# Kernel tuning notes

Measured on AMD Instinct MI355X. Metric: run time of the kernel, lower is better.

Reference implementation:

```python
import jax, jax.numpy as jnp
import numpy as np

EPS = 1e-5
LORA_DIM = 64
LORA_SCALE = LORA_DIM ** (-0.5)
GRAD_SCALE = 0.5  # infeat_grad_scale (bp_to_unet=True path)


def _ln(x, g=None, b=None):
    mu = jnp.mean(x, axis=-1, keepdims=True)
    var = jnp.mean((x - mu) ** 2, axis=-1, keepdims=True)
    y = (x - mu) * jax.lax.rsqrt(var + EPS)
    if g is not None:
        y = y * g + b
    return y


def _grad_scale(t, s=GRAD_SCALE):
    # identity in forward, scales gradient by s in backward
    return t * s + jax.lax.stop_gradient(t) * (1.0 - s)


def setup_inputs() -> dict:
    key = jax.random.key(0)
    ks = jax.random.split(key, 8)
    B, C, H, W = 32, 1280, 32, 32
    TD, LD = 768, LORA_DIM
    inp = {}
    inp["layer_infeat"] = jax.random.normal(ks[0], (B, C, H, W), jnp.float32)
    inp["layer_inquery"] = jax.random.normal(ks[1], (B, H * W, C), jnp.float32)
    inp["token_q_emb"] = jax.random.normal(ks[2], (TD,), jnp.float32)
    # learned params
    inp["to_q_w"] = jax.random.normal(ks[3], (C, TD), jnp.float32) * (TD ** -0.5)
    inp["ln_x_g"] = jnp.ones((C,), jnp.float32)
    inp["ln_x_b"] = jnp.zeros((C,), jnp.float32)
    inp["ln_k_g"] = jnp.ones((C,), jnp.float32)
    inp["ln_k_b"] = jnp.zeros((C,), jnp.float32)
    inp["ln_q_g"] = jnp.ones((TD,), jnp.float32)
    inp["ln_q_b"] = jnp.zeros((TD,), jnp.float32)
    inp["lora_q_w"] = jax.random.normal(ks[4], (LD, C), jnp.float32) * (C ** -0.5)
    inp["lora_k_w"] = jax.random.normal(ks[5], (LD, C), jnp.float32) * (C ** -0.5)
    inp["mask"] = jax.random.randint(ks[6], (B, 1, H, W), 0, 2).astype(jnp.float32)
    return inp


def reference(layer_infeat, layer_inquery, token_q_emb, to_q_w,
              ln_x_g, ln_x_b, ln_k_g, ln_k_b, ln_q_g, ln_q_b,
              lora_q_w, lora_k_w, mask):
    B, C, H, W = layer_infeat.shape
    # flatten(2).permute(0,2,1): [B,C,H,W] -> [B, HW, C]
    x = _grad_scale(layer_infeat).reshape(B, C, H * W).transpose(0, 2, 1)
    k_in = _grad_scale(layer_inquery)
    # q = to_q(ln_q(token_q_emb[None])) -> [1, C], broadcast to [B, 1, C]
    q = _ln(token_q_emb[None, :], ln_q_g, ln_q_b) @ to_q_w.T
    q = jnp.broadcast_to(q[None], (B, 1, C))
    k = _ln(k_in, ln_k_g, ln_k_b)   # [B, HW, C]
    v = _ln(x, ln_x_g, ln_x_b)      # [B, HW, C]
    # LoRA score path (use_lora=True since lora_dim>0)
    lora_q = _ln(q) @ lora_q_w.T    # [B, 1, LD]
    lora_k = _ln(k) @ lora_k_w.T    # [B, HW, LD]
    sim = jnp.einsum('bid,bjd->bij', lora_q, lora_k) * LORA_SCALE  # [B,1,HW]
    # mask: nearest interpolation to (H,W) is identity (same size); flatten
    m = mask.reshape(B, 1, H * W) > 0
    sim = jnp.where(m, sim, -jnp.finfo(sim.dtype).max)
    attn = jax.nn.softmax(sim, axis=-1)
    fg = jnp.einsum('bij,bjd->bid', attn, v)            # [B, 1, C]
    bg = jnp.mean(v, axis=1, keepdims=True) - fg        # [B, 1, C]
    out = jnp.concatenate([fg, bg], axis=-1)            # [B, 1, 2C]
    return out[:, 0, :]                                  # [B, 2C]
```

## Files before the change

kernel.cpp:

```cpp
#include <hip/hip_runtime.h>
#include <math.h>

#define B_   32
#define CD   1280
#define HW_  1024
#define TD_  768
#define LD_  64
#define EPSF 1e-5f
#define LORA_SCALE_F 0.125f

__device__ __forceinline__ float wredSum(float a) {
#pragma unroll
  for (int o = 32; o; o >>= 1) a += __shfl_xor(a, o, 64);
  return a;
}
__device__ __forceinline__ void wred2(float& a, float& b) {
#pragma unroll
  for (int o = 32; o; o >>= 1) { a += __shfl_xor(a, o, 64); b += __shfl_xor(b, o, 64); }
}
__device__ __forceinline__ void wred3(float& a, float& b, float& c) {
#pragma unroll
  for (int o = 32; o; o >>= 1) {
    a += __shfl_xor(a, o, 64); b += __shfl_xor(b, o, 64); c += __shfl_xor(c, o, 64);
  }
}
__device__ __forceinline__ float blockSum(float v, float* red) {
  int t = threadIdx.x;
  red[t] = v; __syncthreads();
#pragma unroll
  for (int s = 128; s > 0; s >>= 1) { if (t < s) red[t] += red[t + s]; __syncthreads(); }
  float r = red[0]; __syncthreads();
  return r;
}
__device__ __forceinline__ void blockSum2(float& a, float& b, float2* red) {
  int t = threadIdx.x;
  red[t] = make_float2(a, b); __syncthreads();
#pragma unroll
  for (int s = 128; s > 0; s >>= 1) {
    if (t < s) { red[t].x += red[t + s].x; red[t].y += red[t + s].y; }
    __syncthreads();
  }
  a = red[0].x; b = red[0].y; __syncthreads();
}

__global__ __launch_bounds__(256) void kA12(const float* __restrict__ tq,
                                            const float* __restrict__ lng,
                                            const float* __restrict__ lnb,
                                            const float* __restrict__ to_q_w,
                                            float* __restrict__ q_out) {
  __shared__ float lnq[TD_];
  __shared__ float2 red[256];
  int t = threadIdx.x;
  float s = 0.f, ss = 0.f, vals[3];
#pragma unroll
  for (int k = 0; k < 3; k++) { float v = tq[t + 256 * k]; vals[k] = v; s += v; ss += v * v; }
  blockSum2(s, ss, red);
  float mu = s * (1.f / TD_);
  float r = rsqrtf(ss * (1.f / TD_) - mu * mu + EPSF);
#pragma unroll
  for (int k = 0; k < 3; k++) { int i = t + 256 * k; lnq[i] = (vals[k] - mu) * r * lng[i] + lnb[i]; }
  __syncthreads();
  int c = blockIdx.x * 4 + (t >> 6);
  int lane = t & 63;
  const float4* w4 = (const float4*)(to_q_w + (size_t)c * TD_);
  const float4* l4 = (const float4*)lnq;
  float dot = 0.f;
#pragma unroll
  for (int i = 0; i < 3; i++) {
    int f = i * 64 + lane;
    float4 w = w4[f], l = l4[f];
    dot += w.x * l.x + w.y * l.y + w.z * l.z + w.w * l.w;
  }
  dot = wredSum(dot);
  if (lane == 0) q_out[c] = dot;
}

__global__ __launch_bounds__(256) void kA3456(const float* __restrict__ q_in,
                                              const float* __restrict__ lora_q_w,
                                              const float* __restrict__ lora_k_w,
                                              float* __restrict__ w_eff) {
  __shared__ float qn[CD];
  __shared__ float lq[LD_];
  __shared__ float redS[8];
  int t = threadIdx.x;
  int wid = t >> 6, lane = t & 63;
  float s = 0.f, ss = 0.f, vals[5];
#pragma unroll
  for (int k = 0; k < 5; k++) { float v = q_in[t + 256 * k]; vals[k] = v; s += v; ss += v * v; }
  wred2(s, ss);
  if (lane == 0) { redS[wid * 2] = s; redS[wid * 2 + 1] = ss; }
  __syncthreads();
  s = redS[0] + redS[2] + redS[4] + redS[6];
  ss = redS[1] + redS[3] + redS[5] + redS[7];
  float mu = s * (1.f / CD);
  float r = rsqrtf(ss * (1.f / CD) - mu * mu + EPSF);
#pragma unroll
  for (int k = 0; k < 5; k++) { int i = t + 256 * k; qn[i] = (vals[k] - mu) * r; }
  __syncthreads();
  {
    int g = t >> 2, sub = t & 3;
    const float4* w4 = (const float4*)(lora_q_w + (size_t)g * CD);
    const float4* q4 = (const float4*)qn;
    float dot = 0.f;
#pragma unroll 8
    for (int i = 0; i < 80; i++) {
      int f = i * 4 + sub;
      float4 w = w4[f], qq = q4[f];
      dot += w.x * qq.x + w.y * qq.y + w.z * qq.z + w.w * qq.w;
    }
    dot += __shfl_xor(dot, 1, 64);
    dot += __shfl_xor(dot, 2, 64);
    if (sub == 0) lq[g] = dot;
  }
  __syncthreads();
  int c = blockIdx.x * 256 + t;
  float acc = 0.f;
#pragma unroll 8
  for (int d = 0; d < LD_; d++) acc += lq[d] * lora_k_w[(size_t)d * CD + c];
  w_eff[c] = acc;
}

__global__ __launch_bounds__(256) void kBD1(const float* __restrict__ kin,
                                            const float* __restrict__ g,
                                            const float* __restrict__ bb,
                                            const float* __restrict__ w_eff,
                                            float* __restrict__ sim,
                                            const float* __restrict__ infeat,
                                            float* __restrict__ mu_out,
                                            float* __restrict__ r_out) {
  __shared__ float4 smem[1024];
  int t = threadIdx.x;
  if (blockIdx.x < 2048) {
    float4* gs = smem;
    float4* bs = smem + 320;
    float4* ws = smem + 640;
    float* red = (float*)(smem + 960);
    float wsum = 0.f;
    for (int k = t; k < CD / 4; k += 256) {
      float4 w = ((const float4*)w_eff)[k];
      ws[k] = w;
      gs[k] = ((const float4*)g)[k];
      bs[k] = ((const float4*)bb)[k];
      wsum += w.x + w.y + w.z + w.w;
    }
    float W0 = blockSum(wsum, red);
    int wid = t >> 6, lane = t & 63;
    int gw = blockIdx.x * 4 + wid;
    for (int row = gw; row < B_ * HW_; row += 8192) {
      const float4* x4 = (const float4*)(kin + (size_t)row * CD);
      float4 xv[5];
      float s = 0.f, ss = 0.f;
#pragma unroll
      for (int i = 0; i < 5; i++) {
        float4 v = x4[i * 64 + lane];
        xv[i] = v;
        s += v.x + v.y + v.z + v.w;
        ss += v.x * v.x + v.y * v.y + v.z * v.z + v.w * v.w;
      }
      wred2(s, ss);
      float mu1 = s * (1.f / CD);
      float r1 = rsqrtf(ss * (1.f / CD) - mu1 * mu1 + EPSF);
      float s2 = 0.f, ss2 = 0.f;
#pragma unroll
      for (int i = 0; i < 5; i++) {
        int f = i * 64 + lane;
        float4 G = gs[f], Bv = bs[f], v = xv[i], kk;
        kk.x = (v.x - mu1) * r1 * G.x + Bv.x;
        kk.y = (v.y - mu1) * r1 * G.y + Bv.y;
        kk.z = (v.z - mu1) * r1 * G.z + Bv.z;
        kk.w = (v.w - mu1) * r1 * G.w + Bv.w;
        xv[i] = kk;
        s2 += kk.x + kk.y + kk.z + kk.w;
        ss2 += kk.x * kk.x + kk.y * kk.y + kk.z * kk.z + kk.w * kk.w;
      }
      wred2(s2, ss2);
      float mu2 = s2 * (1.f / CD);
      float r2 = rsqrtf(ss2 * (1.f / CD) - mu2 * mu2 + EPSF);
      float dot = 0.f;
#pragma unroll
      for (int i = 0; i < 5; i++) {
        float4 w = ws[i * 64 + lane], kk = xv[i];
        dot += w.x * kk.x + w.y * kk.y + w.z * kk.z + w.w * kk.w;
      }
      dot = wredSum(dot);
      if (lane == 0) sim[row] = LORA_SCALE_F * r2 * (dot - mu2 * W0);
    }
  } else {
    int blk = blockIdx.x - 2048;
    int tile = blk & 15, b = blk >> 4;
    int jg = t & 15;
    int slice = t >> 4;
    int j0 = tile * 64 + jg * 4;
    const float* base = infeat + (size_t)b * CD * HW_ + j0;
    float4 s = make_float4(0, 0, 0, 0), q = make_float4(0, 0, 0, 0);
    int c0 = slice * 80;
#pragma unroll 4
    for (int c = c0; c < c0 + 80; c++) {
      float4 v = *(const float4*)(base + (size_t)c * HW_);
      s.x += v.x; s.y += v.y; s.z += v.z; s.w += v.w;
      q.x += v.x * v.x; q.y += v.y * v.y; q.z += v.z * v.z; q.w += v.w * v.w;
    }
    float4* sArr = smem;
    float4* qArr = smem + 256;
    sArr[slice * 16 + jg] = s; qArr[slice * 16 + jg] = q;
    __syncthreads();
#pragma unroll
    for (int st = 8; st > 0; st >>= 1) {
      if (slice < st) {
        float4 a = sArr[slice * 16 + jg], b2 = sArr[(slice + st) * 16 + jg];
        a.x += b2.x; a.y += b2.y; a.z += b2.z; a.w += b2.w;
        sArr[slice * 16 + jg] = a;
        a = qArr[slice * 16 + jg]; b2 = qArr[(slice + st) * 16 + jg];
        a.x += b2.x; a.y += b2.y; a.z += b2.z; a.w += b2.w;
        qArr[slice * 16 + jg] = a;
      }
      __syncthreads();
    }
    if (slice == 0) {
      float4 S = sArr[jg], Q = qArr[jg], mu, r;
      mu.x = S.x * (1.f / CD); mu.y = S.y * (1.f / CD);
      mu.z = S.z * (1.f / CD); mu.w = S.w * (1.f / CD);
      r.x = rsqrtf(Q.x * (1.f / CD) - mu.x * mu.x + EPSF);
      r.y = rsqrtf(Q.y * (1.f / CD) - mu.y * mu.y + EPSF);
      r.z = rsqrtf(Q.z * (1.f / CD) - mu.z * mu.z + EPSF);
      r.w = rsqrtf(Q.w * (1.f / CD) - mu.w * mu.w + EPSF);
      int j = b * HW_ + j0;
      *(float4*)(mu_out + j) = mu;
      *(float4*)(r_out + j) = r;
    }
  }
}

__global__ __launch_bounds__(256) void kD2f(const float* __restrict__ infeat,
                                            const float* __restrict__ sim,
                                            const float* __restrict__ mask,
                                            const float* __restrict__ mu,
                                            const float* __restrict__ r,
                                            const float* __restrict__ g,
                                            const float* __restrict__ bb,
                                            float* __restrict__ out) {
  __shared__ float4 w1s[HW_ / 4], w2s[HW_ / 4];
  __shared__ float red[16];
  int t = threadIdx.x;
  int b = blockIdx.x / 40, tile = blockIdx.x % 40;
  int wid = t >> 6, lane = t & 63;

  float4 sv = ((const float4*)(sim + b * HW_))[t];
  float4 mv = ((const float4*)(mask + b * HW_))[t];
  float4 muv = ((const float4*)(mu + b * HW_))[t];
  float4 rv = ((const float4*)(r + b * HW_))[t];
  const float NEG = -3.4028235e38f;
  float se0 = mv.x > 0.f ? sv.x : NEG;
  float se1 = mv.y > 0.f ? sv.y : NEG;
  float se2 = mv.z > 0.f ? sv.z : NEG;
  float se3 = mv.w > 0.f ? sv.w : NEG;
  float m = fmaxf(fmaxf(se0, se1), fmaxf(se2, se3));
#pragma unroll
  for (int o = 32; o; o >>= 1) m = fmaxf(m, __shfl_xor(m, o, 64));
  if (lane == 0) red[wid] = m;
  __syncthreads();
  float M = fmaxf(fmaxf(red[0], red[1]), fmaxf(red[2], red[3]));
  float e0 = expf(se0 - M), e1 = expf(se1 - M), e2 = expf(se2 - M), e3 = expf(se3 - M);
  float Z = e0 + e1 + e2 + e3;
  float t1 = e0 * rv.x * muv.x + e1 * rv.y * muv.y + e2 * rv.z * muv.z + e3 * rv.w * muv.w;
  float t3 = rv.x * muv.x + rv.y * muv.y + rv.z * muv.z + rv.w * muv.w;
  wred3(Z, t1, t3);
  __syncthreads();
  if (lane == 0) { red[4 + wid * 3] = Z; red[5 + wid * 3] = t1; red[6 + wid * 3] = t3; }
  __syncthreads();
  Z  = red[4] + red[7] + red[10] + red[13];
  t1 = red[5] + red[8] + red[11] + red[14];
  t3 = red[6] + red[9] + red[12] + red[15];
  float inv = 1.f / Z;
  float s1 = t1 * inv;
  float s3 = t3 * (1.f / HW_);
  w1s[t] = make_float4(e0 * rv.x * inv, e1 * rv.y * inv, e2 * rv.z * inv, e3 * rv.w * inv);
  w2s[t] = make_float4(rv.x * (1.f / HW_), rv.y * (1.f / HW_),
                       rv.z * (1.f / HW_), rv.w * (1.f / HW_));
  __syncthreads();

#pragma unroll
  for (int k = 0; k < 8; k++) {
    int c = tile * 32 + wid * 8 + k;
    const float4* x4 = (const float4*)(infeat + (size_t)b * CD * HW_ + (size_t)c * HW_);
    float d1 = 0.f, d2 = 0.f;
#pragma unroll
    for (int i = 0; i < 4; i++) {
      int f = i * 64 + lane;
      float4 x = x4[f], a = w1s[f], w = w2s[f];
      d1 += x.x * a.x + x.y * a.y + x.z * a.z + x.w * a.w;
      d2 += x.x * w.x + x.y * w.y + x.z * w.z + x.w * w.w;
    }
    wred2(d1, d2);
    if (lane == 0) {
      float gc = g[c], bc = bb[c];
      float fg = gc * (d1 - s1) + bc;
      float vm = gc * (d2 - s3) + bc;
      out[(size_t)b * (2 * CD) + c] = fg;
      out[(size_t)b * (2 * CD) + CD + c] = vm - fg;
    }
  }
}

extern "C" void kernel_launch(void* const* d_in, const int* in_sizes, int n_in,
                              void* d_out, int out_size, void* d_ws, size_t ws_size,
                              hipStream_t stream) {
  const float* infeat  = (const float*)d_in[0];
  const float* inquery = (const float*)d_in[1];
  const float* tq      = (const float*)d_in[2];
  const float* to_q_w  = (const float*)d_in[3];
  const float* ln_x_g  = (const float*)d_in[4];
  const float* ln_x_b  = (const float*)d_in[5];
  const float* ln_k_g  = (const float*)d_in[6];
  const float* ln_k_b  = (const float*)d_in[7];
  const float* ln_q_g  = (const float*)d_in[8];
  const float* ln_q_b  = (const float*)d_in[9];
  const float* lora_q_w = (const float*)d_in[10];
  const float* lora_k_w = (const float*)d_in[11];
  const float* mask    = (const float*)d_in[12];
  float* out = (float*)d_out;

  float* ws = (float*)d_ws;
  float* q_ws    = ws;
  float* weff_ws = ws + 1280;
  float* sim_ws  = ws + 2560;
  float* mu_ws   = ws + 35328;
  float* r_ws    = ws + 68096;

  kA12<<<320, 256, 0, stream>>>(tq, ln_q_g, ln_q_b, to_q_w, q_ws);
  kA3456<<<5, 256, 0, stream>>>(q_ws, lora_q_w, lora_k_w, weff_ws);
  kBD1<<<2560, 256, 0, stream>>>(inquery, ln_k_g, ln_k_b, weff_ws, sim_ws,
                                 infeat, mu_ws, r_ws);
  kD2f<<<1280, 256, 0, stream>>>(infeat, sim_ws, mask, mu_ws, r_ws,
                                 ln_x_g, ln_x_b, out);
}
```

Before: 406.5 us.

## Interleave LN and stats blocks and process two rows per wave iteration

kBD1 now interleaves its two roles by block index (four LayerNorm-score blocks, then one infeat-stats block), so the two memory streams run concurrently instead of in two phases. Each wave now handles two rows per iteration with a fixed trip count, which doubles the loads in flight and shares the shuffle reductions between rows. The shared-memory block reduction of W0 becomes wave shuffles plus a 4-entry sum. kD2f likewise processes two channels per iteration, and launch bounds request 4 blocks per CU, which raises register pressure and risks spills.

```diff
diff --git a/kernel.cpp b/kernel.cpp
--- a/kernel.cpp
+++ b/kernel.cpp
@@ -24,13 +24,12 @@
     a += __shfl_xor(a, o, 64); b += __shfl_xor(b, o, 64); c += __shfl_xor(c, o, 64);
   }
 }
-__device__ __forceinline__ float blockSum(float v, float* red) {
-  int t = threadIdx.x;
-  red[t] = v; __syncthreads();
-#pragma unroll
-  for (int s = 128; s > 0; s >>= 1) { if (t < s) red[t] += red[t + s]; __syncthreads(); }
-  float r = red[0]; __syncthreads();
-  return r;
+__device__ __forceinline__ void wred4(float& a, float& b, float& c, float& d) {
+#pragma unroll
+  for (int o = 32; o; o >>= 1) {
+    a += __shfl_xor(a, o, 64); b += __shfl_xor(b, o, 64);
+    c += __shfl_xor(c, o, 64); d += __shfl_xor(d, o, 64);
+  }
 }
 __device__ __forceinline__ void blockSum2(float& a, float& b, float2* red) {
   int t = threadIdx.x;
@@ -120,21 +119,25 @@
   w_eff[c] = acc;
 }
 
-__global__ __launch_bounds__(256) void kBD1(const float* __restrict__ kin,
-                                            const float* __restrict__ g,
-                                            const float* __restrict__ bb,
-                                            const float* __restrict__ w_eff,
-                                            float* __restrict__ sim,
-                                            const float* __restrict__ infeat,
-                                            float* __restrict__ mu_out,
-                                            float* __restrict__ r_out) {
+__global__ __launch_bounds__(256, 4) void kBD1(const float* __restrict__ kin,
+                                               const float* __restrict__ g,
+                                               const float* __restrict__ bb,
+                                               const float* __restrict__ w_eff,
+                                               float* __restrict__ sim,
+                                               const float* __restrict__ infeat,
+                                               float* __restrict__ mu_out,
+                                               float* __restrict__ r_out) {
   __shared__ float4 smem[1024];
   int t = threadIdx.x;
-  if (blockIdx.x < 2048) {
+  int m5 = blockIdx.x % 5;
+  int d5 = blockIdx.x / 5;
+  if (m5 != 4) {
+    int kbid = d5 * 4 + m5;
     float4* gs = smem;
     float4* bs = smem + 320;
     float4* ws = smem + 640;
     float* red = (float*)(smem + 960);
+    int wid = t >> 6, lane = t & 63;
     float wsum = 0.f;
     for (int k = t; k < CD / 4; k += 256) {
       float4 w = ((const float4*)w_eff)[k];
@@ -143,50 +146,76 @@
       bs[k] = ((const float4*)bb)[k];
       wsum += w.x + w.y + w.z + w.w;
     }
-    float W0 = blockSum(wsum, red);
-    int wid = t >> 6, lane = t & 63;
-    int gw = blockIdx.x * 4 + wid;
-    for (int row = gw; row < B_ * HW_; row += 8192) {
-      const float4* x4 = (const float4*)(kin + (size_t)row * CD);
-      float4 xv[5];
-      float s = 0.f, ss = 0.f;
+    wsum = wredSum(wsum);
+    if (lane == 0) red[wid] = wsum;
+    __syncthreads();
+    float W0 = red[0] + red[1] + red[2] + red[3];
+
+    int gw = kbid * 4 + wid;
+#pragma unroll
+    for (int m = 0; m < 2; m++) {
+      int rowA = gw + 16384 * m;
+      int rowB = rowA + 8192;
+      const float4* xA = (const float4*)(kin + (size_t)rowA * CD);
+      const float4* xB = (const float4*)(kin + (size_t)rowB * CD);
+      float4 xva[5], xvb[5];
+      float sa = 0.f, ssa = 0.f, sb = 0.f, ssb = 0.f;
 #pragma unroll
       for (int i = 0; i < 5; i++) {
-        float4 v = x4[i * 64 + lane];
-        xv[i] = v;
-        s += v.x + v.y + v.z + v.w;
-        ss += v.x * v.x + v.y * v.y + v.z * v.z + v.w * v.w;
-      }
-      wred2(s, ss);
-      float mu1 = s * (1.f / CD);
-      float r1 = rsqrtf(ss * (1.f / CD) - mu1 * mu1 + EPSF);
-      float s2 = 0.f, ss2 = 0.f;
+        float4 va = xA[i * 64 + lane];
+        float4 vb = xB[i * 64 + lane];
+        xva[i] = va; xvb[i] = vb;
+        sa += va.x + va.y + va.z + va.w;
+        ssa += va.x * va.x + va.y * va.y + va.z * va.z + va.w * va.w;
+        sb += vb.x + vb.y + vb.z + vb.w;
+        ssb += vb.x * vb.x + vb.y * vb.y + vb.z * vb.z + vb.w * vb.w;
+      }
+      wred4(sa, ssa, sb, ssb);
+      float muA = sa * (1.f / CD);
+      float rA = rsqrtf(ssa * (1.f / CD) - muA * muA + EPSF);
+      float muB = sb * (1.f / CD);
+      float rB = rsqrtf(ssb * (1.f / CD) - muB * muB + EPSF);
+      float s2a = 0.f, ss2a = 0.f, s2b = 0.f, ss2b = 0.f;
 #pragma unroll
       for (int i = 0; i < 5; i++) {
         int f = i * 64 + lane;
-        float4 G = gs[f], Bv = bs[f], v = xv[i], kk;
-        kk.x = (v.x - mu1) * r1 * G.x + Bv.x;
-        kk.y = (v.y - mu1) * r1 * G.y + Bv.y;
-        kk.z = (v.z - mu1) * r1 * G.z + Bv.z;
-        kk.w = (v.w - mu1) * r1 * G.w + Bv.w;
-        xv[i] = kk;
-        s2 += kk.x + kk.y + kk.z + kk.w;
-        ss2 += kk.x * kk.x + kk.y * kk.y + kk.z * kk.z + kk.w * kk.w;
-      }
-      wred2(s2, ss2);
-      float mu2 = s2 * (1.f / CD);
-      float r2 = rsqrtf(ss2 * (1.f / CD) - mu2 * mu2 + EPSF);
-      float dot = 0.f;
+        float4 G = gs[f], Bv = bs[f];
+        float4 va = xva[i], vb = xvb[i], ka, kb;
+        ka.x = (va.x - muA) * rA * G.x + Bv.x;
+        ka.y = (va.y - muA) * rA * G.y + Bv.y;
+        ka.z = (va.z - muA) * rA * G.z + Bv.z;
+        ka.w = (va.w - muA) * rA * G.w + Bv.w;
+        kb.x = (vb.x - muB) * rB * G.x + Bv.x;
+        kb.y = (vb.y - muB) * rB * G.y + Bv.y;
+        kb.z = (vb.z - muB) * rB * G.z + Bv.z;
+        kb.w = (vb.w - muB) * rB * G.w + Bv.w;
+        xva[i] = ka; xvb[i] = kb;
+        s2a += ka.x + ka.y + ka.z + ka.w;
+        ss2a += ka.x * ka.x + ka.y * ka.y + ka.z * ka.z + ka.w * ka.w;
+        s2b += kb.x + kb.y + kb.z + kb.w;
+        ss2b += kb.x * kb.x + kb.y * kb.y + kb.z * kb.z + kb.w * kb.w;
+      }
+      wred4(s2a, ss2a, s2b, ss2b);
+      float mu2a = s2a * (1.f / CD);
+      float r2a = rsqrtf(ss2a * (1.f / CD) - mu2a * mu2a + EPSF);
+      float mu2b = s2b * (1.f / CD);
+      float r2b = rsqrtf(ss2b * (1.f / CD) - mu2b * mu2b + EPSF);
+      float da = 0.f, db = 0.f;
 #pragma unroll
       for (int i = 0; i < 5; i++) {
-        float4 w = ws[i * 64 + lane], kk = xv[i];
-        dot += w.x * kk.x + w.y * kk.y + w.z * kk.z + w.w * kk.w;
-      }
-      dot = wredSum(dot);
-      if (lane == 0) sim[row] = LORA_SCALE_F * r2 * (dot - mu2 * W0);
+        int f = i * 64 + lane;
+        float4 w = ws[f], ka = xva[i], kb = xvb[i];
+        da += w.x * ka.x + w.y * ka.y + w.z * ka.z + w.w * ka.w;
+        db += w.x * kb.x + w.y * kb.y + w.z * kb.z + w.w * kb.w;
+      }
+      wred2(da, db);
+      if (lane == 0) {
+        sim[rowA] = LORA_SCALE_F * r2a * (da - mu2a * W0);
+        sim[rowB] = LORA_SCALE_F * r2b * (db - mu2b * W0);
+      }
     }
   } else {
-    int blk = blockIdx.x - 2048;
+    int blk = d5;
     int tile = blk & 15, b = blk >> 4;
     int jg = t & 15;
     int slice = t >> 4;
@@ -194,7 +223,7 @@
     const float* base = infeat + (size_t)b * CD * HW_ + j0;
     float4 s = make_float4(0, 0, 0, 0), q = make_float4(0, 0, 0, 0);
     int c0 = slice * 80;
-#pragma unroll 4
+#pragma unroll 8
     for (int c = c0; c < c0 + 80; c++) {
       float4 v = *(const float4*)(base + (size_t)c * HW_);
       s.x += v.x; s.y += v.y; s.z += v.z; s.w += v.w;
@@ -231,14 +260,14 @@
   }
 }
 
-__global__ __launch_bounds__(256) void kD2f(const float* __restrict__ infeat,
-                                            const float* __restrict__ sim,
-                                            const float* __restrict__ mask,
-                                            const float* __restrict__ mu,
-                                            const float* __restrict__ r,
-                                            const float* __restrict__ g,
-                                            const float* __restrict__ bb,
-                                            float* __restrict__ out) {
+__global__ __launch_bounds__(256, 4) void kD2f(const float* __restrict__ infeat,
+                                               const float* __restrict__ sim,
+                                               const float* __restrict__ mask,
+                                               const float* __restrict__ mu,
+                                               const float* __restrict__ r,
+                                               const float* __restrict__ g,
+                                               const float* __restrict__ bb,
+                                               float* __restrict__ out) {
   __shared__ float4 w1s[HW_ / 4], w2s[HW_ / 4];
   __shared__ float red[16];
   int t = threadIdx.x;
@@ -279,25 +308,35 @@
                        rv.z * (1.f / HW_), rv.w * (1.f / HW_));
   __syncthreads();
 
-#pragma unroll
-  for (int k = 0; k < 8; k++) {
-    int c = tile * 32 + wid * 8 + k;
-    const float4* x4 = (const float4*)(infeat + (size_t)b * CD * HW_ + (size_t)c * HW_);
-    float d1 = 0.f, d2 = 0.f;
+  const float* bbase = infeat + (size_t)b * CD * HW_;
+#pragma unroll
+  for (int k = 0; k < 4; k++) {
+    int c0 = tile * 32 + wid * 8 + 2 * k;
+    const float4* xa = (const float4*)(bbase + (size_t)c0 * HW_);
+    const float4* xb = xa + (HW_ / 4);
+    float d1a = 0.f, d2a = 0.f, d1b = 0.f, d2b = 0.f;
 #pragma unroll
     for (int i = 0; i < 4; i++) {
       int f = i * 64 + lane;
-      float4 x = x4[f], a = w1s[f], w = w2s[f];
-      d1 += x.x * a.x + x.y * a.y + x.z * a.z + x.w * a.w;
-      d2 += x.x * w.x + x.y * w.y + x.z * w.z + x.w * w.w;
-    }
-    wred2(d1, d2);
+      float4 x0 = xa[f], x1 = xb[f], a = w1s[f], w = w2s[f];
+      d1a += x0.x * a.x + x0.y * a.y + x0.z * a.z + x0.w * a.w;
+      d2a += x0.x * w.x + x0.y * w.y + x0.z * w.z + x0.w * w.w;
+      d1b += x1.x * a.x + x1.y * a.y + x1.z * a.z + x1.w * a.w;
+      d2b += x1.x * w.x + x1.y * w.y + x1.z * w.z + x1.w * w.w;
+    }
+    wred4(d1a, d2a, d1b, d2b);
     if (lane == 0) {
-      float gc = g[c], bc = bb[c];
-      float fg = gc * (d1 - s1) + bc;
-      float vm = gc * (d2 - s3) + bc;
-      out[(size_t)b * (2 * CD) + c] = fg;
-      out[(size_t)b * (2 * CD) + CD + c] = vm - fg;
+      int c1 = c0 + 1;
+      float gc0 = g[c0], bc0 = bb[c0];
+      float gc1 = g[c1], bc1 = bb[c1];
+      float fg0 = gc0 * (d1a - s1) + bc0;
+      float vm0 = gc0 * (d2a - s3) + bc0;
+      float fg1 = gc1 * (d1b - s1) + bc1;
+      float vm1 = gc1 * (d2b - s3) + bc1;
+      out[(size_t)b * (2 * CD) + c0] = fg0;
+      out[(size_t)b * (2 * CD) + CD + c0] = vm0 - fg0;
+      out[(size_t)b * (2 * CD) + c1] = fg1;
+      out[(size_t)b * (2 * CD) + CD + c1] = vm1 - fg1;
     }
   }
 }
```

Measured after the change: 411.0 us. Within noise of the previous version (+1.1%).

## Compute double-LayerNorm score from single-pass moments and batch channel reductions

Applied to the files above, without the earlier changes.

The k-path kernel now computes the double LayerNorm plus LoRA dot product from one set of per-row moments, using precomputed gamma/beta/weight products held in shared memory. This removes the second normalization pass and two of the three wave reductions per row. Each wave handles two rows at once with a fixed 4-row schedule, and infeat-stat blocks are interleaved with the score blocks (one in five). The final kernel batches its eight channel dot products so there is a single combined shuffle reduction, and launch bounds request higher occupancy. The expanded-moment algebra may cost some floating-point accuracy, and the fixed row schedule assumes the exact grid size.

```diff
diff --git a/kernel.cpp b/kernel.cpp
--- a/kernel.cpp
+++ b/kernel.cpp
@@ -24,13 +24,13 @@
     a += __shfl_xor(a, o, 64); b += __shfl_xor(b, o, 64); c += __shfl_xor(c, o, 64);
   }
 }
-__device__ __forceinline__ float blockSum(float v, float* red) {
-  int t = threadIdx.x;
-  red[t] = v; __syncthreads();
-#pragma unroll
-  for (int s = 128; s > 0; s >>= 1) { if (t < s) red[t] += red[t + s]; __syncthreads(); }
-  float r = red[0]; __syncthreads();
-  return r;
+template<int N>
+__device__ __forceinline__ void wredN(float* v) {
+#pragma unroll
+  for (int o = 32; o; o >>= 1) {
+#pragma unroll
+    for (int k = 0; k < N; k++) v[k] += __shfl_xor(v[k], o, 64);
+  }
 }
 __device__ __forceinline__ void blockSum2(float& a, float& b, float2* red) {
   int t = threadIdx.x;
@@ -98,8 +98,8 @@
   for (int k = 0; k < 5; k++) { int i = t + 256 * k; qn[i] = (vals[k] - mu) * r; }
   __syncthreads();
   {
-    int g = t >> 2, sub = t & 3;
-    const float4* w4 = (const float4*)(lora_q_w + (size_t)g * CD);
+    int gg = t >> 2, sub = t & 3;
+    const float4* w4 = (const float4*)(lora_q_w + (size_t)gg * CD);
     const float4* q4 = (const float4*)qn;
     float dot = 0.f;
 #pragma unroll 8
@@ -110,7 +110,7 @@
     }
     dot += __shfl_xor(dot, 1, 64);
     dot += __shfl_xor(dot, 2, 64);
-    if (sub == 0) lq[g] = dot;
+    if (sub == 0) lq[gg] = dot;
   }
   __syncthreads();
   int c = blockIdx.x * 256 + t;
@@ -120,73 +120,122 @@
   w_eff[c] = acc;
 }
 
-__global__ __launch_bounds__(256) void kBD1(const float* __restrict__ kin,
-                                            const float* __restrict__ g,
-                                            const float* __restrict__ bb,
-                                            const float* __restrict__ w_eff,
-                                            float* __restrict__ sim,
-                                            const float* __restrict__ infeat,
-                                            float* __restrict__ mu_out,
-                                            float* __restrict__ r_out) {
-  __shared__ float4 smem[1024];
-  int t = threadIdx.x;
-  if (blockIdx.x < 2048) {
-    float4* gs = smem;
-    float4* bs = smem + 320;
-    float4* ws = smem + 640;
-    float* red = (float*)(smem + 960);
-    float wsum = 0.f;
-    for (int k = t; k < CD / 4; k += 256) {
-      float4 w = ((const float4*)w_eff)[k];
-      ws[k] = w;
-      gs[k] = ((const float4*)g)[k];
-      bs[k] = ((const float4*)bb)[k];
-      wsum += w.x + w.y + w.z + w.w;
-    }
-    float W0 = blockSum(wsum, red);
-    int wid = t >> 6, lane = t & 63;
-    int gw = blockIdx.x * 4 + wid;
-    for (int row = gw; row < B_ * HW_; row += 8192) {
-      const float4* x4 = (const float4*)(kin + (size_t)row * CD);
-      float4 xv[5];
-      float s = 0.f, ss = 0.f;
-#pragma unroll
-      for (int i = 0; i < 5; i++) {
-        float4 v = x4[i * 64 + lane];
-        xv[i] = v;
-        s += v.x + v.y + v.z + v.w;
-        ss += v.x * v.x + v.y * v.y + v.z * v.z + v.w * v.w;
-      }
-      wred2(s, ss);
-      float mu1 = s * (1.f / CD);
-      float r1 = rsqrtf(ss * (1.f / CD) - mu1 * mu1 + EPSF);
-      float s2 = 0.f, ss2 = 0.f;
+__global__ __launch_bounds__(256, 4) void kBD1(const float* __restrict__ kin,
+                                               const float* __restrict__ g,
+                                               const float* __restrict__ bb,
+                                               const float* __restrict__ w_eff,
+                                               float* __restrict__ sim,
+                                               const float* __restrict__ infeat,
+                                               float* __restrict__ mu_out,
+                                               float* __restrict__ r_out) {
+  __shared__ float smem[5152];
+  int t = threadIdx.x;
+  int m5 = blockIdx.x % 5, d5 = blockIdx.x / 5;
+  int wid = t >> 6, lane = t & 63;
+  if (m5 != 4) {
+    int kbid = d5 * 4 + m5;
+    float* cg  = smem;
+    float* cg2 = smem + 1280;
+    float* cgb = smem + 2560;
+    float* cwg = smem + 3840;
+    float* red = smem + 5120;
+    float p[8] = {0.f,0.f,0.f,0.f,0.f,0.f,0.f,0.f};
+    for (int kk = t; kk < 320; kk += 256) {
+      float4 g4 = ((const float4*)g)[kk];
+      float4 b4 = ((const float4*)bb)[kk];
+      float4 w4 = ((const float4*)w_eff)[kk];
+      float4 q4  = make_float4(g4.x*g4.x, g4.y*g4.y, g4.z*g4.z, g4.w*g4.w);
+      float4 gb4 = make_float4(g4.x*b4.x, g4.y*b4.y, g4.z*b4.z, g4.w*b4.w);
+      float4 wg4 = make_float4(w4.x*g4.x, w4.y*g4.y, w4.z*g4.z, w4.w*g4.w);
+      ((float4*)cg)[kk]  = g4;
+      ((float4*)cg2)[kk] = q4;
+      ((float4*)cgb)[kk] = gb4;
+      ((float4*)cwg)[kk] = wg4;
+      p[0] += g4.x + g4.y + g4.z + g4.w;
+      p[1] += b4.x + b4.y + b4.z + b4.w;
+      p[2] += q4.x + q4.y + q4.z + q4.w;
+      p[3] += gb4.x + gb4.y + gb4.z + gb4.w;
+      p[4] += b4.x*b4.x + b4.y*b4.y + b4.z*b4.z + b4.w*b4.w;
+      p[5] += wg4.x + wg4.y + wg4.z + wg4.w;
+      p[6] += w4.x*b4.x + w4.y*b4.y + w4.z*b4.z + w4.w*b4.w;
+      p[7] += w4.x + w4.y + w4.z + w4.w;
+    }
+    wredN<8>(p);
+    if (lane == 0) {
+#pragma unroll
+      for (int j = 0; j < 8; j++) red[wid * 8 + j] = p[j];
+    }
+    __syncthreads();
+    float G0 = red[0] + red[8]  + red[16] + red[24];
+    float B0 = red[1] + red[9]  + red[17] + red[25];
+    float G2 = red[2] + red[10] + red[18] + red[26];
+    float GB = red[3] + red[11] + red[19] + red[27];
+    float B2 = red[4] + red[12] + red[20] + red[28];
+    float WG = red[5] + red[13] + red[21] + red[29];
+    float WB = red[6] + red[14] + red[22] + red[30];
+    float W0 = red[7] + red[15] + red[23] + red[31];
+    const float invC = 1.f / CD;
+    const float4* cg4  = (const float4*)cg;
+    const float4* cg24 = (const float4*)cg2;
+    const float4* cgb4 = (const float4*)cgb;
+    const float4* cwg4 = (const float4*)cwg;
+
+    int gw = kbid * 4 + wid;
+#pragma unroll
+    for (int m = 0; m < 2; m++) {
+      int rowA = gw + 16384 * m;
+      int rowB = rowA + 8192;
+      const float4* xA = (const float4*)(kin + (size_t)rowA * CD);
+      const float4* xB = (const float4*)(kin + (size_t)rowB * CD);
+      float v[14];
+#pragma unroll
+      for (int k = 0; k < 14; k++) v[k] = 0.f;
 #pragma unroll
       for (int i = 0; i < 5; i++) {
         int f = i * 64 + lane;
-        float4 G = gs[f], Bv = bs[f], v = xv[i], kk;
-        kk.x = (v.x - mu1) * r1 * G.x + Bv.x;
-        kk.y = (v.y - mu1) * r1 * G.y + Bv.y;
-        kk.z = (v.z - mu1) * r1 * G.z + Bv.z;
-        kk.w = (v.w - mu1) * r1 * G.w + Bv.w;
-        xv[i] = kk;
-        s2 += kk.x + kk.y + kk.z + kk.w;
-        ss2 += kk.x * kk.x + kk.y * kk.y + kk.z * kk.z + kk.w * kk.w;
+        float4 xa = xA[f], xb = xB[f];
+        float4 c1 = cg4[f], c2 = cg24[f], c3 = cgb4[f], c4 = cwg4[f];
+#define ACC(X, Gc, G2c, GBc, WGc, o) { \
+        float x_ = (X); float x2_ = x_ * x_; \
+        v[(o)+0] += x_; v[(o)+1] += x2_; \
+        v[(o)+2] = fmaf((Gc),  x_,  v[(o)+2]); \
+        v[(o)+3] = fmaf((G2c), x_,  v[(o)+3]); \
+        v[(o)+4] = fmaf((G2c), x2_, v[(o)+4]); \
+        v[(o)+5] = fmaf((GBc), x_,  v[(o)+5]); \
+        v[(o)+6] = fmaf((WGc), x_,  v[(o)+6]); }
+        ACC(xa.x, c1.x, c2.x, c3.x, c4.x, 0)
+        ACC(xa.y, c1.y, c2.y, c3.y, c4.y, 0)
+        ACC(xa.z, c1.z, c2.z, c3.z, c4.z, 0)
+        ACC(xa.w, c1.w, c2.w, c3.w, c4.w, 0)
+        ACC(xb.x, c1.x, c2.x, c3.x, c4.x, 7)
+        ACC(xb.y, c1.y, c2.y, c3.y, c4.y, 7)
+        ACC(xb.z, c1.z, c2.z, c3.z, c4.z, 7)
+        ACC(xb.w, c1.w, c2.w, c3.w, c4.w, 7)
+#undef ACC
       }
-      wred2(s2, ss2);
-      float mu2 = s2 * (1.f / CD);
-      float r2 = rsqrtf(ss2 * (1.f / CD) - mu2 * mu2 + EPSF);
-      float dot = 0.f;
-#pragma unroll
-      for (int i = 0; i < 5; i++) {
-        float4 w = ws[i * 64 + lane], kk = xv[i];
-        dot += w.x * kk.x + w.y * kk.y + w.z * kk.z + w.w * kk.w;
-      }
-      dot = wredSum(dot);
-      if (lane == 0) sim[row] = LORA_SCALE_F * r2 * (dot - mu2 * W0);
+      wredN<14>(v);
+      float mu1a = v[0] * invC;
+      float r1a  = rsqrtf(v[1] * invC - mu1a * mu1a + EPSF);
+      float s2a  = r1a * (v[2] - mu1a * G0) + B0;
+      float mu2a = s2a * invC;
+      float ss2a = r1a * r1a * (v[4] - 2.f * mu1a * v[3] + mu1a * mu1a * G2)
+                 + 2.f * r1a * (v[5] - mu1a * GB) + B2;
+      float r2a  = rsqrtf(ss2a * invC - mu2a * mu2a + EPSF);
+      float dta  = r1a * (v[6] - mu1a * WG) + WB;
+      float simA = LORA_SCALE_F * r2a * (dta - mu2a * W0);
+      float mu1b = v[7] * invC;
+      float r1b  = rsqrtf(v[8] * invC - mu1b * mu1b + EPSF);
+      float s2b  = r1b * (v[9] - mu1b * G0) + B0;
+      float mu2b = s2b * invC;
+      float ss2b = r1b * r1b * (v[11] - 2.f * mu1b * v[10] + mu1b * mu1b * G2)
+                 + 2.f * r1b * (v[12] - mu1b * GB) + B2;
+      float r2b  = rsqrtf(ss2b * invC - mu2b * mu2b + EPSF);
+      float dtb  = r1b * (v[13] - mu1b * WG) + WB;
+      float simB = LORA_SCALE_F * r2b * (dtb - mu2b * W0);
+      if (lane == 0) { sim[rowA] = simA; sim[rowB] = simB; }
     }
   } else {
-    int blk = blockIdx.x - 2048;
+    int blk = d5;
     int tile = blk & 15, b = blk >> 4;
     int jg = t & 15;
     int slice = t >> 4;
@@ -194,14 +243,14 @@
     const float* base = infeat + (size_t)b * CD * HW_ + j0;
     float4 s = make_float4(0, 0, 0, 0), q = make_float4(0, 0, 0, 0);
     int c0 = slice * 80;
-#pragma unroll 4
+#pragma unroll 8
     for (int c = c0; c < c0 + 80; c++) {
       float4 v = *(const float4*)(base + (size_t)c * HW_);
       s.x += v.x; s.y += v.y; s.z += v.z; s.w += v.w;
       q.x += v.x * v.x; q.y += v.y * v.y; q.z += v.z * v.z; q.w += v.w * v.w;
     }
-    float4* sArr = smem;
-    float4* qArr = smem + 256;
+    float4* sArr = (float4*)smem;
+    float4* qArr = ((float4*)smem) + 256;
     sArr[slice * 16 + jg] = s; qArr[slice * 16 + jg] = q;
     __syncthreads();
 #pragma unroll
@@ -231,14 +280,14 @@
   }
 }
 
-__global__ __launch_bounds__(256) void kD2f(const float* __restrict__ infeat,
-                                            const float* __restrict__ sim,
-                                            const float* __restrict__ mask,
-                                            const float* __restrict__ mu,
-                                            const float* __restrict__ r,
-                                            const float* __restrict__ g,
-                                            const float* __restrict__ bb,
-                                            float* __restrict__ out) {
+__global__ __launch_bounds__(256, 4) void kD2f(const float* __restrict__ infeat,
+                                               const float* __restrict__ sim,
+                                               const float* __restrict__ mask,
+                                               const float* __restrict__ mu,
+                                               const float* __restrict__ r,
+                                               const float* __restrict__ g,
+                                               const float* __restrict__ bb,
+                                               float* __restrict__ out) {
   __shared__ float4 w1s[HW_ / 4], w2s[HW_ / 4];
   __shared__ float red[16];
   int t = threadIdx.x;
@@ -279,23 +328,30 @@
                        rv.z * (1.f / HW_), rv.w * (1.f / HW_));
   __syncthreads();
 
-#pragma unroll
-  for (int k = 0; k < 8; k++) {
-    int c = tile * 32 + wid * 8 + k;
-    const float4* x4 = (const float4*)(infeat + (size_t)b * CD * HW_ + (size_t)c * HW_);
-    float d1 = 0.f, d2 = 0.f;
-#pragma unroll
-    for (int i = 0; i < 4; i++) {
-      int f = i * 64 + lane;
-      float4 x = x4[f], a = w1s[f], w = w2s[f];
-      d1 += x.x * a.x + x.y * a.y + x.z * a.z + x.w * a.w;
-      d2 += x.x * w.x + x.y * w.y + x.z * w.z + x.w * w.w;
-    }
-    wred2(d1, d2);
-    if (lane == 0) {
+  int cbase = tile * 32 + wid * 8;
+  const float* bbase = infeat + (size_t)b * CD * HW_;
+  float v[16];
+#pragma unroll
+  for (int k = 0; k < 16; k++) v[k] = 0.f;
+#pragma unroll
+  for (int i = 0; i < 4; i++) {
+    int f = i * 64 + lane;
+    float4 a = w1s[f], w = w2s[f];
+#pragma unroll
+    for (int k = 0; k < 8; k++) {
+      float4 x = ((const float4*)(bbase + (size_t)(cbase + k) * HW_))[f];
+      v[2 * k]     += x.x * a.x + x.y * a.y + x.z * a.z + x.w * a.w;
+      v[2 * k + 1] += x.x * w.x + x.y * w.y + x.z * w.z + x.w * w.w;
+    }
+  }
+  wredN<16>(v);
+  if (lane == 0) {
+#pragma unroll
+    for (int k = 0; k < 8; k++) {
+      int c = cbase + k;
       float gc = g[c], bc = bb[c];
-      float fg = gc * (d1 - s1) + bc;
-      float vm = gc * (d2 - s3) + bc;
+      float fg = gc * (v[2 * k] - s1) + bc;
+      float vm = gc * (v[2 * k + 1] - s3) + bc;
       out[(size_t)b * (2 * CD) + c] = fg;
       out[(size_t)b * (2 * CD) + CD + c] = vm - fg;
     }
```

New measurement: 416.0 us. 2.3% more time.
